# Kernel tuning notes

Measured on AMD Instinct MI355X. Metric: run time of the kernel, lower is better.

Reference implementation:

```python
import jax, jax.numpy as jnp
import numpy as np

BN_EPS = 1e-5

def setup_inputs() -> dict:
    key = jax.random.key(0)
    ks = jax.random.split(key, 6)
    N, C, T, V = 64, 64, 300, 25
    Ci, Co, S = 16, 64, 3  # inter_channels = out//4, num_subset = 3
    x = jax.random.normal(ks[0], (N, C, T, V), dtype=jnp.float32)
    # static (non-trainable) adjacency buffer; graph_attn is init.constant_(1)
    A_static = jax.random.uniform(ks[1], (S, V, V), dtype=jnp.float32)
    graph_attn = jnp.ones((S, V, V), jnp.float32)
    # stacked 1x1 conv weights for the 3 subsets: (S, out_c, in_c)
    Wg = jax.random.normal(ks[2], (S, Co, C), jnp.float32) * 0.05
    bg = jnp.zeros((S, Co), jnp.float32)
    Wa = jax.random.normal(ks[3], (S, Ci, C), jnp.float32) * 0.05
    ba = jnp.zeros((S, Ci), jnp.float32)
    Wb = jax.random.normal(ks[4], (S, Ci, C), jnp.float32) * 0.05
    bb = jnp.zeros((S, Ci), jnp.float32)
    # BatchNorm2d (eval mode: running stats)
    gamma = jnp.ones((Co,), jnp.float32)
    beta = jnp.zeros((Co,), jnp.float32)
    run_mean = jnp.zeros((Co,), jnp.float32)
    run_var = jnp.ones((Co,), jnp.float32)
    return {"x": x, "A_static": A_static, "graph_attn": graph_attn,
            "Wg": Wg, "bg": bg, "Wa": Wa, "ba": ba, "Wb": Wb, "bb": bb,
            "gamma": gamma, "beta": beta, "run_mean": run_mean, "run_var": run_var}

def _conv1x1(x, W, b):
    # x: (N,C,T,V), W: (O,C), b: (O,) -> (N,O,T,V)
    return jnp.einsum('nctv,oc->notv', x, W) + b[None, :, None, None]

def reference(x, A_static, graph_attn, Wg, bg, Wa, ba, Wb, bb, gamma, beta, run_mean, run_var):
    N, C, T, V = x.shape
    Ci = Wa.shape[1]
    A = A_static + graph_attn            # (3, V, V)
    x_flat = x.reshape(N, C * T, V)
    hidden = jnp.zeros((), x.dtype)
    for i in range(Wg.shape[0]):
        a = _conv1x1(x, Wa[i], ba[i])                                  # (N,Ci,T,V)
        b2 = _conv1x1(x, Wb[i], bb[i])                                 # (N,Ci,T,V)
        A1 = a.transpose(0, 3, 1, 2).reshape(N, V, Ci * T)             # (N,V,Ci*T)
        A2 = b2.reshape(N, Ci * T, V)                                  # (N,Ci*T,V)
        attn = jax.nn.softmax(jnp.matmul(A1, A2) / (Ci * T), axis=-2)  # softmax over dim -2
        attn = attn + A[i]                                             # (N,V,V)
        y = jnp.matmul(x_flat, attn).reshape(N, C, T, V)
        hidden = hidden + _conv1x1(y, Wg[i], bg[i])
    inv = (gamma / jnp.sqrt(run_var + BN_EPS))[None, :, None, None]
    hn = (hidden - run_mean[None, :, None, None]) * inv + beta[None, :, None, None]
    return jax.nn.relu(hn + x)  # in_channels == out_channels -> identity residual
```

## Files before the change

kernel.cpp:

```cpp
#include <hip/hip_runtime.h>

typedef unsigned short u16;
typedef __attribute__((ext_vector_type(8))) short short8;
typedef __attribute__((ext_vector_type(4))) unsigned short ushort4v;
typedef __attribute__((ext_vector_type(4))) float float4v;

#define TVB 7500
#define CTVB 480000

static __device__ __forceinline__ float bf2f(u16 a) {
    union { unsigned u; float f; } x; x.u = ((unsigned)a) << 16; return x.f;
}
static __device__ __forceinline__ u16 f2bf(float f) {
    union { float f; unsigned u; } x; x.f = f;
    unsigned r = x.u + 0x7fffu + ((x.u >> 16) & 1u);
    return (u16)(r >> 16);
}

__global__ __launch_bounds__(256, 3) void kA(
    const float* __restrict__ xg, const float* __restrict__ Wa, const float* __restrict__ ba,
    const float* __restrict__ Wb, const float* __restrict__ bb, float* __restrict__ Sws)
{
    __shared__ u16 xT[4][32][72];
    __shared__ u16 asT[3][32][72];
    __shared__ u16 bsT[3][32][72];
    const int tid  = threadIdx.x;
    const int lane = tid & 63;
    const int w    = tid >> 6;
    const int l15  = lane & 15;
    const int q    = lane >> 4;
    const int n    = blockIdx.y;
    const int t0   = blockIdx.x * 20;

    for (int e = tid; e < 4 * 7 * 72; e += 256) {
        int tt = e / (7 * 72);
        int r  = e - tt * (7 * 72);
        xT[tt][25 + r / 72][r % 72] = 0;
    }

    int tts[3], iis[3];
    #pragma unroll
    for (int m = 0; m < 3; ++m) { int u = w + 4 * m; tts[m] = u / 3; iis[m] = u - 3 * tts[m]; }

    short8 waf[3][2], wbf[3][2];
    float ba_r[3][4], bb_r[3][4];
    #pragma unroll
    for (int m = 0; m < 3; ++m) {
        const int i = iis[m];
        const float* wap = Wa + i * 1024;
        const float* wbp = Wb + i * 1024;
        #pragma unroll
        for (int kf = 0; kf < 2; ++kf) {
            short8 fa, fb;
            int base = l15 * 64 + kf * 32 + q * 8;
            #pragma unroll
            for (int j = 0; j < 8; ++j) {
                fa[j] = (short)f2bf(wap[base + j]);
                fb[j] = (short)f2bf(wbp[base + j]);
            }
            waf[m][kf] = fa; wbf[m][kf] = fb;
        }
        #pragma unroll
        for (int r = 0; r < 4; ++r) {
            ba_r[m][r] = ba[i * 16 + q * 4 + r];
            bb_r[m][r] = bb[i * 16 + q * 4 + r];
        }
    }

    float4v accS[3];
    #pragma unroll
    for (int i = 0; i < 3; ++i) accS[i] = (float4v){0.f, 0.f, 0.f, 0.f};

    const float* xb = xg + (size_t)n * CTVB;

    for (int g = 0; g < 5; ++g) {
        __syncthreads();
        for (int e = tid; e < 1600; e += 256) {
            int c = e / 25;
            int j = e - c * 25;
            float4v xv = *(const float4v*)(xb + (size_t)c * TVB + (t0 + g * 4) * 25 + j * 4);
            #pragma unroll
            for (int k2 = 0; k2 < 4; ++k2) {
                int idx = j * 4 + k2;
                int tt = idx / 25;
                int uu = idx - tt * 25;
                xT[tt][uu][c] = f2bf(xv[k2]);
            }
        }
        __syncthreads();
        #pragma unroll
        for (int m = 0; m < 3; ++m) {
            const int tt = tts[m];
            const int i  = iis[m];
            float4v aA0 = {0,0,0,0}, aA1 = {0,0,0,0}, aB0 = {0,0,0,0}, aB1 = {0,0,0,0};
            #pragma unroll
            for (int kf = 0; kf < 2; ++kf) {
                short8 x0 = *(const short8*)&xT[tt][l15][kf * 32 + q * 8];
                short8 x1 = *(const short8*)&xT[tt][16 + l15][kf * 32 + q * 8];
                aA0 = __builtin_amdgcn_mfma_f32_16x16x32_bf16(waf[m][kf], x0, aA0, 0, 0, 0);
                aA1 = __builtin_amdgcn_mfma_f32_16x16x32_bf16(waf[m][kf], x1, aA1, 0, 0, 0);
                aB0 = __builtin_amdgcn_mfma_f32_16x16x32_bf16(wbf[m][kf], x0, aB0, 0, 0, 0);
                aB1 = __builtin_amdgcn_mfma_f32_16x16x32_bf16(wbf[m][kf], x1, aB1, 0, 0, 0);
            }
            ushort4v pa0, pa1, pb0, pb1;
            #pragma unroll
            for (int r = 0; r < 4; ++r) {
                pa0[r] = f2bf(aA0[r] + ba_r[m][r]);
                pa1[r] = f2bf(aA1[r] + ba_r[m][r]);
                pb0[r] = f2bf(aB0[r] + bb_r[m][r]);
                pb1[r] = f2bf(aB1[r] + bb_r[m][r]);
            }
            int kb = tt * 16 + q * 4;
            *(ushort4v*)&asT[i][l15][kb]      = pa0;
            *(ushort4v*)&asT[i][16 + l15][kb] = pa1;
            *(ushort4v*)&bsT[i][l15][kb]      = pb0;
            *(ushort4v*)&bsT[i][16 + l15][kb] = pb1;
        }
        __syncthreads();
        const int mt = w >> 1, nt = w & 1;
        #pragma unroll
        for (int i = 0; i < 3; ++i) {
            #pragma unroll
            for (int ks = 0; ks < 2; ++ks) {
                short8 af  = *(const short8*)&asT[i][mt * 16 + l15][ks * 32 + q * 8];
                short8 bf_ = *(const short8*)&bsT[i][nt * 16 + l15][ks * 32 + q * 8];
                accS[i] = __builtin_amdgcn_mfma_f32_16x16x32_bf16(af, bf_, accS[i], 0, 0, 0);
            }
        }
    }
    const int mt = w >> 1, nt = w & 1;
    #pragma unroll
    for (int i = 0; i < 3; ++i) {
        #pragma unroll
        for (int r = 0; r < 4; ++r) {
            int u = mt * 16 + q * 4 + r;
            int v = nt * 16 + l15;
            if (u < 25 && v < 25)
                atomicAdd(&Sws[(i * 64 + n) * 625 + u * 25 + v], accS[i][r]);
        }
    }
}

__global__ __launch_bounds__(64) void kS(float* __restrict__ Sws,
    const float* __restrict__ Ast, const float* __restrict__ Gat)
{
    int g = blockIdx.x;
    int i = g >> 6;
    int v = threadIdx.x;
    if (v >= 25) return;
    float vals[25];
    float m = -1e30f;
    #pragma unroll
    for (int u = 0; u < 25; ++u) {
        float s = Sws[g * 625 + u * 25 + v] * (1.0f / 4800.0f);
        vals[u] = s;
        m = fmaxf(m, s);
    }
    float sum = 0.f;
    #pragma unroll
    for (int u = 0; u < 25; ++u) { float e = __expf(vals[u] - m); vals[u] = e; sum += e; }
    float isum = 1.f / sum;
    #pragma unroll
    for (int u = 0; u < 25; ++u) {
        int idx = i * 625 + u * 25 + v;
        Sws[g * 625 + u * 25 + v] = vals[u] * isum + Ast[idx] + Gat[idx];
    }
}

__global__ __launch_bounds__(256, 4) void kB(
    const float* __restrict__ xg, const float* __restrict__ Wgp, const float* __restrict__ bgp,
    const float* __restrict__ gam, const float* __restrict__ bet, const float* __restrict__ rmu,
    const float* __restrict__ rva, const float* __restrict__ attnw, float* __restrict__ outg)
{
    __shared__ u16 xsu[4][64][40];
    __shared__ u16 ysT[32][200];
    __shared__ u16 pTs[3][32][32];
    const int tid  = threadIdx.x;
    const int lane = tid & 63;
    const int w    = tid >> 6;
    const int l15  = lane & 15;
    const int q    = lane >> 4;
    const int n    = blockIdx.y;
    const int t0   = blockIdx.x * 4;

    for (int e = tid; e < 3 * 32 * 32; e += 256) ((u16*)pTs)[e] = 0;
    const float* xb = xg + (size_t)n * CTVB;
    for (int e = tid; e < 1600; e += 256) {
        int c = e / 25;
        int j = e - c * 25;
        float4v xv = *(const float4v*)(xb + (size_t)c * TVB + t0 * 25 + j * 4);
        #pragma unroll
        for (int k = 0; k < 4; ++k) {
            int idx = j * 4 + k;
            int tt = idx / 25;
            int u  = idx - tt * 25;
            xsu[tt][c][u] = f2bf(xv[k]);
        }
    }
    for (int e = tid; e < 4 * 64 * 7; e += 256) {
        int tt = e / (64 * 7);
        int r  = e - tt * (64 * 7);
        xsu[tt][r / 7][25 + r % 7] = 0;
    }
    __syncthreads();
    for (int e = tid; e < 1875; e += 256) {
        int i = e / 625;
        int r = e - i * 625;
        int u = r / 25;
        int v = r - u * 25;
        pTs[i][v][u] = f2bf(attnw[(i * 64 + n) * 625 + r]);
    }
    short8 wgf[6];
    const int o_row = w * 16 + l15;
    #pragma unroll
    for (int kf = 0; kf < 6; ++kf) {
        int i  = kf >> 1;
        int c0 = (kf & 1) * 32 + q * 8;
        const float* p = Wgp + i * 4096 + o_row * 64 + c0;
        short8 f;
        #pragma unroll
        for (int j = 0; j < 8; ++j) f[j] = (short)f2bf(p[j]);
        wgf[kf] = f;
    }
    float invr[4], add0r[4];
    #pragma unroll
    for (int r = 0; r < 4; ++r) {
        int o = w * 16 + q * 4 + r;
        float gv = gam[o], bt = bet[o], mu = rmu[o], vv = rva[o];
        float bgs = bgp[o] + bgp[64 + o] + bgp[128 + o];
        float iv = gv * rsqrtf(vv + 1e-5f);
        invr[r] = iv;
        add0r[r] = (bgs - mu) * iv + bt;
    }
    __syncthreads();
    short8 pf[3][2];
    #pragma unroll
    for (int i = 0; i < 3; ++i)
        #pragma unroll
        for (int nt = 0; nt < 2; ++nt)
            pf[i][nt] = *(const short8*)&pTs[i][nt * 16 + l15][q * 8];

    for (int tl = 0; tl < 4; ++tl) {
        short8 xf = *(const short8*)&xsu[tl][w * 16 + l15][q * 8];
        #pragma unroll
        for (int i = 0; i < 3; ++i) {
            #pragma unroll
            for (int nt = 0; nt < 2; ++nt) {
                float4v acc = {0, 0, 0, 0};
                acc = __builtin_amdgcn_mfma_f32_16x16x32_bf16(xf, pf[i][nt], acc, 0, 0, 0);
                ushort4v pk;
                #pragma unroll
                for (int r = 0; r < 4; ++r) pk[r] = f2bf(acc[r]);
                *(ushort4v*)&ysT[nt * 16 + l15][i * 64 + w * 16 + q * 4] = pk;
            }
        }
        __syncthreads();
        #pragma unroll
        for (int nt = 0; nt < 2; ++nt) {
            float4v acc = {0, 0, 0, 0};
            #pragma unroll
            for (int kf = 0; kf < 6; ++kf) {
                short8 yf = *(const short8*)&ysT[nt * 16 + l15][kf * 32 + q * 8];
                acc = __builtin_amdgcn_mfma_f32_16x16x32_bf16(wgf[kf], yf, acc, 0, 0, 0);
            }
            int v = nt * 16 + l15;
            if (v < 25) {
                size_t ob = (size_t)n * CTVB + (size_t)(t0 + tl) * 25 + v;
                #pragma unroll
                for (int r = 0; r < 4; ++r) {
                    int o = w * 16 + q * 4 + r;
                    float xres = bf2f(xsu[tl][o][v]);
                    float val = fmaf(acc[r], invr[r], add0r[r]) + xres;
                    val = fmaxf(val, 0.f);
                    outg[ob + (size_t)o * TVB] = val;
                }
            }
        }
        __syncthreads();
    }
}

extern "C" void kernel_launch(void* const* d_in, const int* in_sizes, int n_in,
                              void* d_out, int out_size, void* d_ws, size_t ws_size,
                              hipStream_t stream) {
    const float* x    = (const float*)d_in[0];
    const float* Ast  = (const float*)d_in[1];
    const float* Gat  = (const float*)d_in[2];
    const float* Wg   = (const float*)d_in[3];
    const float* bg   = (const float*)d_in[4];
    const float* Wa   = (const float*)d_in[5];
    const float* ba   = (const float*)d_in[6];
    const float* Wb   = (const float*)d_in[7];
    const float* bb   = (const float*)d_in[8];
    const float* gam  = (const float*)d_in[9];
    const float* bet  = (const float*)d_in[10];
    const float* rmu  = (const float*)d_in[11];
    const float* rva  = (const float*)d_in[12];
    float* out = (float*)d_out;
    float* Sws = (float*)d_ws;

    hipMemsetAsync(Sws, 0, 192 * 625 * sizeof(float), stream);
    kA<<<dim3(15, 64), 256, 0, stream>>>(x, Wa, ba, Wb, bb, Sws);
    kS<<<dim3(192), 64, 0, stream>>>(Sws, Ast, Gat);
    kB<<<dim3(75, 64), 256, 0, stream>>>(x, Wg, bg, gam, bet, rmu, rva, Sws, out);
}
```

Baseline: 361.0 us.

## Emit padded bf16 copy of x in kA and consume it in new kB2

kA now also writes a bf16, channel-major, padded copy of x into workspace, so the final kernel (kB2) reads half the bytes and needs no transpose or LDS staging of x. kA's projection work is restructured so 3 waves each own one subset across all 4 time steps, leaving the fourth wave idle during that phase. kB2 processes 12 time steps per block, cutting block count and reloads of attention and weights. The cost is an extra ~78MB write of xpad, and the path only runs when the workspace is large enough.

```diff
diff --git a/kernel.cpp b/kernel.cpp
--- a/kernel.cpp
+++ b/kernel.cpp
@@ -7,6 +7,8 @@
 
 #define TVB 7500
 #define CTVB 480000
+#define XPAD_OFF 524288
+#define XPAD_U16 39321600ull
 
 static __device__ __forceinline__ float bf2f(u16 a) {
     union { unsigned u; float f; } x; x.u = ((unsigned)a) << 16; return x.f;
@@ -19,7 +21,8 @@
 
 __global__ __launch_bounds__(256, 3) void kA(
     const float* __restrict__ xg, const float* __restrict__ Wa, const float* __restrict__ ba,
-    const float* __restrict__ Wb, const float* __restrict__ bb, float* __restrict__ Sws)
+    const float* __restrict__ Wb, const float* __restrict__ bb, float* __restrict__ Sws,
+    u16* __restrict__ xpad)
 {
     __shared__ u16 xT[4][32][72];
     __shared__ u16 asT[3][32][72];
@@ -31,6 +34,7 @@
     const int q    = lane >> 4;
     const int n    = blockIdx.y;
     const int t0   = blockIdx.x * 20;
+    const bool emit = (xpad != nullptr);
 
     for (int e = tid; e < 4 * 7 * 72; e += 256) {
         int tt = e / (7 * 72);
@@ -38,17 +42,11 @@
         xT[tt][25 + r / 72][r % 72] = 0;
     }
 
-    int tts[3], iis[3];
-    #pragma unroll
-    for (int m = 0; m < 3; ++m) { int u = w + 4 * m; tts[m] = u / 3; iis[m] = u - 3 * tts[m]; }
-
-    short8 waf[3][2], wbf[3][2];
-    float ba_r[3][4], bb_r[3][4];
-    #pragma unroll
-    for (int m = 0; m < 3; ++m) {
-        const int i = iis[m];
-        const float* wap = Wa + i * 1024;
-        const float* wbp = Wb + i * 1024;
+    short8 waf[2], wbf[2];
+    float ba_r[4], bb_r[4];
+    if (w < 3) {
+        const float* wap = Wa + w * 1024;
+        const float* wbp = Wb + w * 1024;
         #pragma unroll
         for (int kf = 0; kf < 2; ++kf) {
             short8 fa, fb;
@@ -58,12 +56,12 @@
                 fa[j] = (short)f2bf(wap[base + j]);
                 fb[j] = (short)f2bf(wbp[base + j]);
             }
-            waf[m][kf] = fa; wbf[m][kf] = fb;
+            waf[kf] = fa; wbf[kf] = fb;
         }
         #pragma unroll
         for (int r = 0; r < 4; ++r) {
-            ba_r[m][r] = ba[i * 16 + q * 4 + r];
-            bb_r[m][r] = bb[i * 16 + q * 4 + r];
+            ba_r[r] = ba[w * 16 + q * 4 + r];
+            bb_r[r] = bb[w * 16 + q * 4 + r];
         }
     }
 
@@ -74,6 +72,7 @@
     const float* xb = xg + (size_t)n * CTVB;
 
     for (int g = 0; g < 5; ++g) {
+        const size_t pbase = ((size_t)n * 300 + t0 + g * 4) * 2048;
         __syncthreads();
         for (int e = tid; e < 1600; e += 256) {
             int c = e / 25;
@@ -84,37 +83,45 @@
                 int idx = j * 4 + k2;
                 int tt = idx / 25;
                 int uu = idx - tt * 25;
-                xT[tt][uu][c] = f2bf(xv[k2]);
-            }
-        }
-        __syncthreads();
-        #pragma unroll
-        for (int m = 0; m < 3; ++m) {
-            const int tt = tts[m];
-            const int i  = iis[m];
-            float4v aA0 = {0,0,0,0}, aA1 = {0,0,0,0}, aB0 = {0,0,0,0}, aB1 = {0,0,0,0};
-            #pragma unroll
-            for (int kf = 0; kf < 2; ++kf) {
-                short8 x0 = *(const short8*)&xT[tt][l15][kf * 32 + q * 8];
-                short8 x1 = *(const short8*)&xT[tt][16 + l15][kf * 32 + q * 8];
-                aA0 = __builtin_amdgcn_mfma_f32_16x16x32_bf16(waf[m][kf], x0, aA0, 0, 0, 0);
-                aA1 = __builtin_amdgcn_mfma_f32_16x16x32_bf16(waf[m][kf], x1, aA1, 0, 0, 0);
-                aB0 = __builtin_amdgcn_mfma_f32_16x16x32_bf16(wbf[m][kf], x0, aB0, 0, 0, 0);
-                aB1 = __builtin_amdgcn_mfma_f32_16x16x32_bf16(wbf[m][kf], x1, aB1, 0, 0, 0);
-            }
-            ushort4v pa0, pa1, pb0, pb1;
-            #pragma unroll
-            for (int r = 0; r < 4; ++r) {
-                pa0[r] = f2bf(aA0[r] + ba_r[m][r]);
-                pa1[r] = f2bf(aA1[r] + ba_r[m][r]);
-                pb0[r] = f2bf(aB0[r] + bb_r[m][r]);
-                pb1[r] = f2bf(aB1[r] + bb_r[m][r]);
-            }
-            int kb = tt * 16 + q * 4;
-            *(ushort4v*)&asT[i][l15][kb]      = pa0;
-            *(ushort4v*)&asT[i][16 + l15][kb] = pa1;
-            *(ushort4v*)&bsT[i][l15][kb]      = pb0;
-            *(ushort4v*)&bsT[i][16 + l15][kb] = pb1;
+                u16 h = f2bf(xv[k2]);
+                xT[tt][uu][c] = h;
+                if (emit) xpad[pbase + (size_t)tt * 2048 + c * 32 + uu] = h;
+            }
+        }
+        if (emit) {
+            int tt = tid >> 6, c = tid & 63;
+            u16* pp = xpad + pbase + (size_t)tt * 2048 + c * 32;
+            #pragma unroll
+            for (int z = 25; z < 32; ++z) pp[z] = 0;
+        }
+        __syncthreads();
+        if (w < 3) {
+            #pragma unroll
+            for (int tt = 0; tt < 4; ++tt) {
+                float4v aA0 = {0,0,0,0}, aA1 = {0,0,0,0}, aB0 = {0,0,0,0}, aB1 = {0,0,0,0};
+                #pragma unroll
+                for (int kf = 0; kf < 2; ++kf) {
+                    short8 x0 = *(const short8*)&xT[tt][l15][kf * 32 + q * 8];
+                    short8 x1 = *(const short8*)&xT[tt][16 + l15][kf * 32 + q * 8];
+                    aA0 = __builtin_amdgcn_mfma_f32_16x16x32_bf16(waf[kf], x0, aA0, 0, 0, 0);
+                    aA1 = __builtin_amdgcn_mfma_f32_16x16x32_bf16(waf[kf], x1, aA1, 0, 0, 0);
+                    aB0 = __builtin_amdgcn_mfma_f32_16x16x32_bf16(wbf[kf], x0, aB0, 0, 0, 0);
+                    aB1 = __builtin_amdgcn_mfma_f32_16x16x32_bf16(wbf[kf], x1, aB1, 0, 0, 0);
+                }
+                ushort4v pa0, pa1, pb0, pb1;
+                #pragma unroll
+                for (int r = 0; r < 4; ++r) {
+                    pa0[r] = f2bf(aA0[r] + ba_r[r]);
+                    pa1[r] = f2bf(aA1[r] + ba_r[r]);
+                    pb0[r] = f2bf(aB0[r] + bb_r[r]);
+                    pb1[r] = f2bf(aB1[r] + bb_r[r]);
+                }
+                int kb = tt * 16 + q * 4;
+                *(ushort4v*)&asT[w][l15][kb]      = pa0;
+                *(ushort4v*)&asT[w][16 + l15][kb] = pa1;
+                *(ushort4v*)&bsT[w][l15][kb]      = pb0;
+                *(ushort4v*)&bsT[w][16 + l15][kb] = pb1;
+            }
         }
         __syncthreads();
         const int mt = w >> 1, nt = w & 1;
@@ -164,6 +171,105 @@
     for (int u = 0; u < 25; ++u) {
         int idx = i * 625 + u * 25 + v;
         Sws[g * 625 + u * 25 + v] = vals[u] * isum + Ast[idx] + Gat[idx];
+    }
+}
+
+__global__ __launch_bounds__(256, 4) void kB2(
+    const float* __restrict__ Wgp, const float* __restrict__ bgp,
+    const float* __restrict__ gam, const float* __restrict__ bet, const float* __restrict__ rmu,
+    const float* __restrict__ rva, const float* __restrict__ attnw, const u16* __restrict__ xpad,
+    float* __restrict__ outg)
+{
+    __shared__ u16 ysT[32][200];
+    __shared__ u16 pTs[3][32][32];
+    const int tid  = threadIdx.x;
+    const int lane = tid & 63;
+    const int w    = tid >> 6;
+    const int l15  = lane & 15;
+    const int q    = lane >> 4;
+    const int n    = blockIdx.y;
+    const int t0   = blockIdx.x * 12;
+
+    for (int e = tid; e < 3 * 32 * 32; e += 256) ((u16*)pTs)[e] = 0;
+    __syncthreads();
+    for (int e = tid; e < 1875; e += 256) {
+        int i = e / 625;
+        int r = e - i * 625;
+        int u = r / 25;
+        int v = r - u * 25;
+        pTs[i][v][u] = f2bf(attnw[(i * 64 + n) * 625 + r]);
+    }
+    short8 wgf[6];
+    const int o_row = w * 16 + l15;
+    #pragma unroll
+    for (int kf = 0; kf < 6; ++kf) {
+        int i  = kf >> 1;
+        int c0 = (kf & 1) * 32 + q * 8;
+        const float* p = Wgp + i * 4096 + o_row * 64 + c0;
+        short8 f;
+        #pragma unroll
+        for (int j = 0; j < 8; ++j) f[j] = (short)f2bf(p[j]);
+        wgf[kf] = f;
+    }
+    float invr[4], add0r[4];
+    #pragma unroll
+    for (int r = 0; r < 4; ++r) {
+        int o = w * 16 + q * 4 + r;
+        float gv = gam[o], bt = bet[o], mu = rmu[o], vv = rva[o];
+        float bgs = bgp[o] + bgp[64 + o] + bgp[128 + o];
+        float iv = gv * rsqrtf(vv + 1e-5f);
+        invr[r] = iv;
+        add0r[r] = (bgs - mu) * iv + bt;
+    }
+    __syncthreads();
+    short8 pf[3][2];
+    #pragma unroll
+    for (int i = 0; i < 3; ++i)
+        #pragma unroll
+        for (int nt = 0; nt < 2; ++nt)
+            pf[i][nt] = *(const short8*)&pTs[i][nt * 16 + l15][q * 8];
+
+    const u16* xpn = xpad + (size_t)n * 300 * 2048;
+    float* ob = outg + (size_t)n * CTVB;
+
+    for (int tl = 0; tl < 12; ++tl) {
+        const int t = t0 + tl;
+        const u16* xp = xpn + (size_t)t * 2048;
+        short8 xf = *(const short8*)&xp[(w * 16 + l15) * 32 + q * 8];
+        #pragma unroll
+        for (int i = 0; i < 3; ++i) {
+            #pragma unroll
+            for (int nt = 0; nt < 2; ++nt) {
+                float4v acc = {0, 0, 0, 0};
+                acc = __builtin_amdgcn_mfma_f32_16x16x32_bf16(xf, pf[i][nt], acc, 0, 0, 0);
+                ushort4v pk;
+                #pragma unroll
+                for (int r = 0; r < 4; ++r) pk[r] = f2bf(acc[r]);
+                *(ushort4v*)&ysT[nt * 16 + l15][i * 64 + w * 16 + q * 4] = pk;
+            }
+        }
+        __syncthreads();
+        #pragma unroll
+        for (int nt = 0; nt < 2; ++nt) {
+            float4v acc = {0, 0, 0, 0};
+            #pragma unroll
+            for (int kf = 0; kf < 6; ++kf) {
+                short8 yf = *(const short8*)&ysT[nt * 16 + l15][kf * 32 + q * 8];
+                acc = __builtin_amdgcn_mfma_f32_16x16x32_bf16(wgf[kf], yf, acc, 0, 0, 0);
+            }
+            int v = nt * 16 + l15;
+            if (v < 25) {
+                #pragma unroll
+                for (int r = 0; r < 4; ++r) {
+                    int o = w * 16 + q * 4 + r;
+                    float xres = bf2f(xp[o * 32 + v]);
+                    float val = fmaf(acc[r], invr[r], add0r[r]) + xres;
+                    val = fmaxf(val, 0.f);
+                    ob[(size_t)o * TVB + t * 25 + v] = val;
+                }
+            }
+        }
+        __syncthreads();
     }
 }
 
@@ -265,14 +371,14 @@
             }
             int v = nt * 16 + l15;
             if (v < 25) {
-                size_t ob = (size_t)n * CTVB + (size_t)(t0 + tl) * 25 + v;
+                size_t obp = (size_t)n * CTVB + (size_t)(t0 + tl) * 25 + v;
                 #pragma unroll
                 for (int r = 0; r < 4; ++r) {
                     int o = w * 16 + q * 4 + r;
                     float xres = bf2f(xsu[tl][o][v]);
                     float val = fmaf(acc[r], invr[r], add0r[r]) + xres;
                     val = fmaxf(val, 0.f);
-                    outg[ob + (size_t)o * TVB] = val;
+                    outg[obp + (size_t)o * TVB] = val;
                 }
             }
         }
@@ -299,8 +405,16 @@
     float* out = (float*)d_out;
     float* Sws = (float*)d_ws;
 
+    const size_t need = (size_t)XPAD_OFF + XPAD_U16 * 2;
     hipMemsetAsync(Sws, 0, 192 * 625 * sizeof(float), stream);
-    kA<<<dim3(15, 64), 256, 0, stream>>>(x, Wa, ba, Wb, bb, Sws);
-    kS<<<dim3(192), 64, 0, stream>>>(Sws, Ast, Gat);
-    kB<<<dim3(75, 64), 256, 0, stream>>>(x, Wg, bg, gam, bet, rmu, rva, Sws, out);
-}
+    if (ws_size >= need) {
+        u16* xpad = (u16*)((char*)d_ws + XPAD_OFF);
+        kA<<<dim3(15, 64), 256, 0, stream>>>(x, Wa, ba, Wb, bb, Sws, xpad);
+        kS<<<dim3(192), 64, 0, stream>>>(Sws, Ast, Gat);
+        kB2<<<dim3(25, 64), 256, 0, stream>>>(Wg, bg, gam, bet, rmu, rva, Sws, xpad, out);
+    } else {
+        kA<<<dim3(15, 64), 256, 0, stream>>>(x, Wa, ba, Wb, bb, Sws, nullptr);
+        kS<<<dim3(192), 64, 0, stream>>>(Sws, Ast, Gat);
+        kB<<<dim3(75, 64), 256, 0, stream>>>(x, Wg, bg, gam, bet, rmu, rva, Sws, out);
+    }
+}
```

Result: slower. 391.3 us (+8.4%).
